# Kernel optimization log

Hardware: AMD Instinct MI355X
Metric: run time of the kernel (lower is better)

## Reference

```python
import jax, jax.numpy as jnp
import numpy as np

B, S, D, H = 4, 2048, 1024, 16
DK = D // H


def setup_inputs() -> dict:
    key = jax.random.key(0)
    ks = jax.random.split(key, 11)
    inp = {
        'query': jax.random.normal(ks[0], (B, S, D), jnp.float32),
        'key': jax.random.normal(ks[1], (B, S, D), jnp.float32),
        'value': jax.random.normal(ks[2], (B, S, D), jnp.float32),
        'mask': jnp.tril(jnp.ones((1, 1, S, S), dtype=bool)),  # causal
    }
    sc = 1.0 / np.sqrt(D)
    inp['w_q'] = jax.random.normal(ks[3], (D, D), jnp.float32) * sc
    inp['b_q'] = jnp.zeros((D,), jnp.float32)
    inp['w_k'] = jax.random.normal(ks[4], (D, D), jnp.float32) * sc
    inp['b_k'] = jnp.zeros((D,), jnp.float32)
    inp['w_v'] = jax.random.normal(ks[5], (D, D), jnp.float32) * sc
    inp['b_v'] = jnp.zeros((D,), jnp.float32)
    inp['w_o'] = jax.random.normal(ks[6], (D, D), jnp.float32) * sc
    inp['b_o'] = jnp.zeros((D,), jnp.float32)
    return inp


def _split_heads(x):
    # Faithful to source: view(B, S, d_k, H) then permute(0,3,1,2)
    b, s, _ = x.shape
    return x.reshape(b, s, DK, H).transpose(0, 3, 1, 2)  # (B, H, S, DK)


def _concat_heads(x):
    # permute(0,2,1,3) -> reshape(B, S, d_k*H)
    b, h, s, dk = x.shape
    return x.transpose(0, 2, 1, 3).reshape(b, s, dk * h)


def reference(query, key, value, mask, w_q, b_q, w_k, b_k, w_v, b_v, w_o, b_o):
    q = query @ w_q.T + b_q
    k = key @ w_k.T + b_k
    v = value @ w_v.T + b_v
    q, k, v = _split_heads(q), _split_heads(k), _split_heads(v)
    scale = 1.0 / jnp.sqrt(jnp.asarray(DK, q.dtype))
    scores = jnp.einsum('bhqd,bhkd->bhqk', q, k) * scale
    scores = jnp.where(mask, scores, -jnp.inf)
    attn = jax.nn.softmax(scores, axis=-1)  # dropout p=0 -> identity
    out = jnp.einsum('bhqk,bhkd->bhqd', attn, v)
    return _concat_heads(out) @ w_o.T + b_o
```

## Files before the change

### kernel.cpp

```cpp
#include <hip/hip_runtime.h>

#define BB 4
#define SS 2048
#define DD 1024
#define HH 16
#define DK 64
#define MM (BB * SS)

typedef __bf16 bf16x8 __attribute__((ext_vector_type(8)));
typedef float f32x4 __attribute__((ext_vector_type(4)));
typedef unsigned short us8 __attribute__((ext_vector_type(8)));
typedef unsigned short us4 __attribute__((ext_vector_type(4)));

#define MFMA_BF16(a, b, c) __builtin_amdgcn_mfma_f32_16x16x32_bf16((a), (b), (c), 0, 0, 0)

__device__ __forceinline__ unsigned short f2bf(float f) {
  return __builtin_bit_cast(unsigned short, (__bf16)f);
}

__device__ __forceinline__ bf16x8 ld_frag(const unsigned short* p) {
  return __builtin_bit_cast(bf16x8, *(const us8*)p);
}

__device__ __forceinline__ void gl_lds16(const unsigned short* g, unsigned short* l) {
  __builtin_amdgcn_global_load_lds((const __attribute__((address_space(1))) void*)g,
                                   (__attribute__((address_space(3))) void*)l, 16, 0, 0);
}

__global__ void cvt_weights(const float* __restrict__ w0, const float* __restrict__ w1,
                            const float* __restrict__ w2, const float* __restrict__ w3,
                            unsigned short* __restrict__ dst) {
  const float* src = (blockIdx.y == 0) ? w0 : (blockIdx.y == 1) ? w1 : (blockIdx.y == 2) ? w2 : w3;
  unsigned short* d = dst + (size_t)blockIdx.y * (DD * DD);
  int idx = (blockIdx.x * 256 + threadIdx.x) * 4;
  float4 v = *(const float4*)(src + idx);
  us4 o;
  o[0] = f2bf(v.x); o[1] = f2bf(v.y); o[2] = f2bf(v.z); o[3] = f2bf(v.w);
  *(us4*)(d + idx) = o;
}

__global__ __launch_bounds__(256, 3) void qkv_gemm(
    const float* __restrict__ xq, const float* __restrict__ xk, const float* __restrict__ xv,
    const unsigned short* __restrict__ wb,
    const float* __restrict__ bq, const float* __restrict__ bk, const float* __restrict__ bv,
    unsigned short* __restrict__ qh, unsigned short* __restrict__ kh,
    unsigned short* __restrict__ vt) {
  const int mode = blockIdx.z;
  const float* x = (mode == 0) ? xq : (mode == 1) ? xk : xv;
  const unsigned short* w = wb + (size_t)mode * (DD * DD);
  const float* bias = (mode == 0) ? bq : (mode == 1) ? bk : bv;

  const int m0 = blockIdx.x * 128;
  const int h0 = blockIdx.y * 2;

  __shared__ unsigned short smem[17408];
  unsigned short* sA = smem;
  unsigned short* sB = smem + 8192;

  const int tid = threadIdx.x;
  const int lane = tid & 63;
  const int wave = tid >> 6;
  const int wm = wave & 1, wn = wave >> 1;
  const int quad = lane >> 4, l16 = lane & 15;

  f32x4 acc[4][4];
#pragma unroll
  for (int i = 0; i < 4; i++)
#pragma unroll
    for (int j = 0; j < 4; j++) acc[i][j] = f32x4{0.f, 0.f, 0.f, 0.f};

  const int arow = tid >> 1, ahalf = tid & 1;
  const float* ag = x + (size_t)(m0 + arow) * DD + ahalf * 32;
  unsigned short* arow_base = sA + ahalf * 4096 + arow * 32;
  const int asw = (arow >> 1) & 3;

  const unsigned short* bsrc[4];
  unsigned short* bdst[4];
#pragma unroll
  for (int j = 0; j < 4; j++) {
    int cid = tid + j * 256;
    int half = cid >> 9, rr = (cid & 511) >> 2, c8 = (cid & 3) << 3;
    int n = ((rr & 63) << 4) + h0 + (rr >> 6);
    bsrc[j] = w + (size_t)n * DD + half * 32 + c8;
    bdst[j] = sB + half * 4096 + rr * 32 + c8;
  }

  float4 va[8];
  us8 vbr[4];
#pragma unroll
  for (int i = 0; i < 8; i++) va[i] = *(const float4*)(ag + 0 + i * 4);
#pragma unroll
  for (int j = 0; j < 4; j++) vbr[j] = *(const us8*)(bsrc[j] + 0);

  for (int k0 = 0; k0 < DD; k0 += 64) {
    __syncthreads();
#pragma unroll
    for (int c = 0; c < 4; c++) {
      us8 o;
      o[0] = f2bf(va[2 * c].x); o[1] = f2bf(va[2 * c].y);
      o[2] = f2bf(va[2 * c].z); o[3] = f2bf(va[2 * c].w);
      o[4] = f2bf(va[2 * c + 1].x); o[5] = f2bf(va[2 * c + 1].y);
      o[6] = f2bf(va[2 * c + 1].z); o[7] = f2bf(va[2 * c + 1].w);
      *(us8*)(arow_base + ((c ^ asw) << 3)) = o;
    }
#pragma unroll
    for (int j = 0; j < 4; j++) *(us8*)(bdst[j]) = vbr[j];
    __syncthreads();

    if (k0 + 64 < DD) {
#pragma unroll
      for (int i = 0; i < 8; i++) va[i] = *(const float4*)(ag + k0 + 64 + i * 4);
#pragma unroll
      for (int j = 0; j < 4; j++) vbr[j] = *(const us8*)(bsrc[j] + k0 + 64);
    }

#pragma unroll
    for (int kk = 0; kk < 2; kk++) {
      bf16x8 af[4];
#pragma unroll
      for (int mi = 0; mi < 4; mi++) {
        int row = wm * 64 + mi * 16 + l16;
        af[mi] = ld_frag(sA + kk * 4096 + row * 32 + ((quad ^ ((row >> 1) & 3)) << 3));
      }
#pragma unroll
      for (int ni = 0; ni < 4; ni++) {
        bf16x8 bfr = ld_frag(sB + kk * 4096 + (wn * 64 + ni * 16 + l16) * 32 + quad * 8);
#pragma unroll
        for (int mi = 0; mi < 4; mi++) acc[mi][ni] = MFMA_BF16(af[mi], bfr, acc[mi][ni]);
      }
    }
  }

  if (mode < 2) {
    unsigned short* outp = (mode == 0) ? qh : kh;
#pragma unroll
    for (int mi = 0; mi < 4; mi++) {
#pragma unroll
      for (int ni = 0; ni < 4; ni++) {
        int c = wn * 64 + ni * 16 + l16;
        int h = h0 + (c >> 6), dk = c & 63;
        float bvv = bias[(dk << 4) + h];
        int mg0 = m0 + wm * 64 + mi * 16 + quad * 4;
#pragma unroll
        for (int r = 0; r < 4; r++) {
          int mg = mg0 + r;
          int bb = mg >> 11, s = mg & 2047;
          size_t dst = ((size_t)((bb << 4) + h) * SS + s) * DK + dk;
          outp[dst] = f2bf(acc[mi][ni][r] + bvv);
        }
      }
    }
  } else {
    __syncthreads();
#pragma unroll
    for (int mi = 0; mi < 4; mi++) {
#pragma unroll
      for (int ni = 0; ni < 4; ni++) {
        int c = wn * 64 + ni * 16 + l16;
        int h = h0 + (c >> 6), dk = c & 63;
        float bvv = bias[(dk << 4) + h];
        int ml0 = wm * 64 + mi * 16 + quad * 4;
#pragma unroll
        for (int r = 0; r < 4; r++)
          smem[c * 136 + ml0 + r] = f2bf(acc[mi][ni][r] + bvv);
      }
    }
    __syncthreads();
    int bb = m0 >> 11;
    int sbase = m0 & 2047;
#pragma unroll
    for (int i = 0; i < 8; i++) {
      int idx = tid + i * 256;
      int c = idx >> 4, mc = (idx & 15) << 3;
      int h = h0 + (c >> 6), dk = c & 63;
      size_t dst = ((size_t)((bb << 4) + h) * DK + dk) * SS + sbase + mc;
      *(us8*)(vt + dst) = *(const us8*)(smem + c * 136 + mc);
    }
  }
}

__global__ __launch_bounds__(256, 2) void attn(
    const unsigned short* __restrict__ qh, const unsigned short* __restrict__ kh,
    const unsigned short* __restrict__ vt, unsigned short* __restrict__ outc) {
  const int bh = blockIdx.x;
  const int by = blockIdx.y;
  const int b = bh >> 4, h = bh & 15;
  const unsigned short* Qp = qh + (size_t)bh * SS * DK;
  const unsigned short* Kp = kh + (size_t)bh * SS * DK;
  const unsigned short* Vp = vt + (size_t)bh * DK * SS;

  __shared__ unsigned short sK[128 * 72];
  __shared__ unsigned short sV[64 * 136];

  const int tid = threadIdx.x;
  const int lane = tid & 63;
  const int wave = tid >> 6;
  const int quad = lane >> 4, l16 = lane & 15;
  const int wq0 = wave * 32;

  const float sl = 0.125f * 1.44269504088896f;

  for (int pass = 0; pass < 2; pass++) {
    const int qt = pass ? (15 - by) : by;
    const int q0 = qt * 128;

    bf16x8 aq[2][2];
#pragma unroll
    for (int mi = 0; mi < 2; mi++)
#pragma unroll
      for (int kk = 0; kk < 2; kk++)
        aq[mi][kk] = ld_frag(Qp + (size_t)(q0 + wq0 + mi * 16 + l16) * DK + kk * 32 + quad * 8);

    f32x4 o_acc[2][4];
    float mrowL[2], lrowL[2];
#pragma unroll
    for (int mi = 0; mi < 2; mi++) {
#pragma unroll
      for (int ni = 0; ni < 4; ni++) o_acc[mi][ni] = f32x4{0.f, 0.f, 0.f, 0.f};
      mrowL[mi] = -1e30f;
      lrowL[mi] = 0.f;
    }

    for (int kt = 0; kt <= qt; kt++) {
      const int k0 = kt * 128;
      const bool diag = (kt == qt);
      __syncthreads();
#pragma unroll
      for (int i = 0; i < 4; i++) {
        int idx = tid + i * 256;
        int row = idx >> 3, c8 = (idx & 7) << 3;
        *(us8*)(sK + row * 72 + c8) = *(const us8*)(Kp + (size_t)(k0 + row) * DK + c8);
      }
#pragma unroll
      for (int i = 0; i < 4; i++) {
        int idx = tid + i * 256;
        int row = idx >> 4, cc = (idx & 15) << 3;
        *(us8*)(sV + row * 136 + cc) = *(const us8*)(Vp + (size_t)row * SS + k0 + cc);
      }
      __syncthreads();

      f32x4 sc[2][8];
#pragma unroll
      for (int mi = 0; mi < 2; mi++)
#pragma unroll
        for (int kti = 0; kti < 8; kti++) sc[mi][kti] = f32x4{0.f, 0.f, 0.f, 0.f};
#pragma unroll
      for (int kti = 0; kti < 8; kti++) {
#pragma unroll
        for (int kk = 0; kk < 2; kk++) {
          bf16x8 ak = ld_frag(sK + (kti * 16 + l16) * 72 + kk * 32 + quad * 8);
#pragma unroll
          for (int mi = 0; mi < 2; mi++) sc[mi][kti] = MFMA_BF16(ak, aq[mi][kk], sc[mi][kti]);
        }
      }

      if (diag) {
#pragma unroll
        for (int mi = 0; mi < 2; mi++) {
          int ql = wq0 + mi * 16 + l16;
#pragma unroll
          for (int kti = 0; kti < 8; kti++)
#pragma unroll
            for (int r = 0; r < 4; r++) {
              int kl = kti * 16 + quad * 4 + r;
              float v = sc[mi][kti][r] * sl;
              sc[mi][kti][r] = (kl > ql) ? -1e30f : v;
            }
        }
      } else {
#pragma unroll
        for (int mi = 0; mi < 2; mi++)
#pragma unroll
          for (int kti = 0; kti < 8; kti++)
#pragma unroll
            for (int r = 0; r < 4; r++) sc[mi][kti][r] *= sl;
      }

      float alphaL[2];
#pragma unroll
      for (int mi = 0; mi < 2; mi++) {
        f32x4 vm = sc[mi][0];
#pragma unroll
        for (int kti = 1; kti < 8; kti++)
#pragma unroll
          for (int r = 0; r < 4; r++) vm[r] = fmaxf(vm[r], sc[mi][kti][r]);
        float mx = fmaxf(fmaxf(vm[0], vm[1]), fmaxf(vm[2], vm[3]));
        mx = fmaxf(mx, __shfl_xor(mx, 16, 64));
        mx = fmaxf(mx, __shfl_xor(mx, 32, 64));
        float mnew = fmaxf(mrowL[mi], mx);
        alphaL[mi] = exp2f(mrowL[mi] - mnew);
        mrowL[mi] = mnew;
      }

#pragma unroll
      for (int mi = 0; mi < 2; mi++) {
#pragma unroll
        for (int r = 0; r < 4; r++) {
          float a = __shfl(alphaL[mi], quad * 4 + r, 64);
#pragma unroll
          for (int ni = 0; ni < 4; ni++) o_acc[mi][ni][r] *= a;
        }
        us4 pk[8];
        f32x4 vs = f32x4{0.f, 0.f, 0.f, 0.f};
#pragma unroll
        for (int kti = 0; kti < 8; kti++) {
#pragma unroll
          for (int r = 0; r < 4; r++) {
            float p = exp2f(sc[mi][kti][r] - mrowL[mi]);
            vs[r] += p;
            pk[kti][r] = f2bf(p);
          }
        }
        float ls = (vs[0] + vs[1]) + (vs[2] + vs[3]);
        ls += __shfl_xor(ls, 16, 64);
        ls += __shfl_xor(ls, 32, 64);
        lrowL[mi] = lrowL[mi] * alphaL[mi] + ls;

#pragma unroll
        for (int c = 0; c < 4; c++) {
          bf16x8 ap = __builtin_bit_cast(
              bf16x8, __builtin_shufflevector(pk[2 * c], pk[2 * c + 1], 0, 1, 2, 3, 4, 5, 6, 7));
#pragma unroll
          for (int ni = 0; ni < 4; ni++) {
            const unsigned short* vb = sV + (ni * 16 + l16) * 136 + c * 32 + quad * 4;
            us4 lo = *(const us4*)vb;
            us4 hi = *(const us4*)(vb + 16);
            bf16x8 bfr = __builtin_bit_cast(
                bf16x8, __builtin_shufflevector(lo, hi, 0, 1, 2, 3, 4, 5, 6, 7));
            o_acc[mi][ni] = MFMA_BF16(ap, bfr, o_acc[mi][ni]);
          }
        }
      }
    }

#pragma unroll
    for (int mi = 0; mi < 2; mi++) {
#pragma unroll
      for (int r = 0; r < 4; r++) {
        float lr = __shfl(lrowL[mi], quad * 4 + r, 64);
        float inv = 1.0f / lr;
        int qg = q0 + wq0 + mi * 16 + quad * 4 + r;
        size_t rowbase = ((size_t)(b * SS + qg)) * DD + h * DK;
#pragma unroll
        for (int ni = 0; ni < 4; ni++) {
          int dk = ni * 16 + l16;
          outc[rowbase + dk] = f2bf(o_acc[mi][ni][r] * inv);
        }
      }
    }
    __syncthreads();
  }
}

__global__ __launch_bounds__(256, 4) void out_proj(
    const unsigned short* __restrict__ ac, const unsigned short* __restrict__ wo,
    const float* __restrict__ bias, float* __restrict__ out) {
  const int m0 = blockIdx.x * 128;
  const int n0 = blockIdx.y * 128;
  __shared__ unsigned short sA[8192];
  __shared__ unsigned short sB[8192];

  const int tid = threadIdx.x;
  const int lane = tid & 63;
  const int wave = tid >> 6;
  const int wm = wave & 1, wn = wave >> 1;
  const int quad = lane >> 4, l16 = lane & 15;

  f32x4 acc[4][4];
#pragma unroll
  for (int i = 0; i < 4; i++)
#pragma unroll
    for (int j = 0; j < 4; j++) acc[i][j] = f32x4{0.f, 0.f, 0.f, 0.f};

  for (int k0 = 0; k0 < DD; k0 += 64) {
    __syncthreads();
#pragma unroll
    for (int j = 0; j < 4; j++) {
      int cid = tid + j * 256;
      int half = cid >> 9;
      int rr = (cid & 511) >> 2;
      int c8 = (cid & 3) << 3;
      gl_lds16(ac + (size_t)(m0 + rr) * DD + k0 + half * 32 + c8,
               sA + half * 4096 + rr * 32 + c8);
    }
#pragma unroll
    for (int j = 0; j < 4; j++) {
      int cid = tid + j * 256;
      int half = cid >> 9;
      int rr = (cid & 511) >> 2;
      int c8 = (cid & 3) << 3;
      gl_lds16(wo + (size_t)(n0 + rr) * DD + k0 + half * 32 + c8,
               sB + half * 4096 + rr * 32 + c8);
    }
    __syncthreads();
#pragma unroll
    for (int kk = 0; kk < 2; kk++) {
      bf16x8 af[4];
#pragma unroll
      for (int mi = 0; mi < 4; mi++)
        af[mi] = ld_frag(sA + kk * 4096 + (wm * 64 + mi * 16 + l16) * 32 + quad * 8);
#pragma unroll
      for (int ni = 0; ni < 4; ni++) {
        bf16x8 bfr = ld_frag(sB + kk * 4096 + (wn * 64 + ni * 16 + l16) * 32 + quad * 8);
#pragma unroll
        for (int mi = 0; mi < 4; mi++) acc[mi][ni] = MFMA_BF16(af[mi], bfr, acc[mi][ni]);
      }
    }
  }

#pragma unroll
  for (int mi = 0; mi < 4; mi++) {
#pragma unroll
    for (int ni = 0; ni < 4; ni++) {
      int n = n0 + wn * 64 + ni * 16 + l16;
      float bvv = bias[n];
      int mg0 = m0 + wm * 64 + mi * 16 + quad * 4;
#pragma unroll
      for (int r = 0; r < 4; r++) out[(size_t)(mg0 + r) * DD + n] = acc[mi][ni][r] + bvv;
    }
  }
}

extern "C" void kernel_launch(void* const* d_in, const int* in_sizes, int n_in,
                              void* d_out, int out_size, void* d_ws, size_t ws_size,
                              hipStream_t stream) {
  const float* q_in = (const float*)d_in[0];
  const float* k_in = (const float*)d_in[1];
  const float* v_in = (const float*)d_in[2];
  const float* w_q = (const float*)d_in[4];
  const float* b_q = (const float*)d_in[5];
  const float* w_k = (const float*)d_in[6];
  const float* b_k = (const float*)d_in[7];
  const float* w_v = (const float*)d_in[8];
  const float* b_v = (const float*)d_in[9];
  const float* w_o = (const float*)d_in[10];
  const float* b_o = (const float*)d_in[11];
  float* out = (float*)d_out;

  unsigned short* ws = (unsigned short*)d_ws;
  unsigned short* wb = ws;
  unsigned short* qh = ws + (size_t)4 * 1024 * 1024;
  unsigned short* kh = ws + (size_t)12 * 1024 * 1024;
  unsigned short* vt = ws + (size_t)20 * 1024 * 1024;
  unsigned short* outc = ws + (size_t)28 * 1024 * 1024;

  const size_t WSZ = (size_t)DD * DD;

  cvt_weights<<<dim3(1024, 4), 256, 0, stream>>>(w_q, w_k, w_v, w_o, wb);
  qkv_gemm<<<dim3(64, 8, 3), 256, 0, stream>>>(q_in, k_in, v_in, wb, b_q, b_k, b_v, qh, kh, vt);
  attn<<<dim3(64, 8), 256, 0, stream>>>(qh, kh, vt, outc);
  out_proj<<<dim3(64, 8), 256, 0, stream>>>(outc, wb + 3 * WSZ, b_o, out);
}
```

Measured before the change: 371.1 us.

## Pre-convert activations to bf16 and load QKV tiles via global_load_lds

Adds a separate kernel that converts the fp32 query/key/value activations to bf16 in workspace buffers, then splits the fused QKV GEMM into three launches that stream bf16 tiles directly into LDS with global_load_lds. This removes the in-loop fp32-to-bf16 conversion and the register staging, but it drops the register prefetch overlap and the LDS swizzle, so bank conflicts and load latency may become exposed. Workspace regions are reused for the converted activations, ordered safely by the sequence of launches on one stream. It also adds s_setprio around the MFMA blocks in attention to favour matrix issue.

```diff
diff --git a/kernel.cpp b/kernel.cpp
--- a/kernel.cpp
+++ b/kernel.cpp
@@ -39,17 +39,23 @@
   *(us4*)(d + idx) = o;
 }
 
-__global__ __launch_bounds__(256, 3) void qkv_gemm(
-    const float* __restrict__ xq, const float* __restrict__ xk, const float* __restrict__ xv,
-    const unsigned short* __restrict__ wb,
-    const float* __restrict__ bq, const float* __restrict__ bk, const float* __restrict__ bv,
-    unsigned short* __restrict__ qh, unsigned short* __restrict__ kh,
-    unsigned short* __restrict__ vt) {
-  const int mode = blockIdx.z;
-  const float* x = (mode == 0) ? xq : (mode == 1) ? xk : xv;
-  const unsigned short* w = wb + (size_t)mode * (DD * DD);
-  const float* bias = (mode == 0) ? bq : (mode == 1) ? bk : bv;
-
+__global__ void cvt_act(const float* __restrict__ xq, const float* __restrict__ xk,
+                        const float* __restrict__ xv, unsigned short* __restrict__ dq,
+                        unsigned short* __restrict__ dk, unsigned short* __restrict__ dv) {
+  const float* src = (blockIdx.y == 0) ? xq : (blockIdx.y == 1) ? xk : xv;
+  unsigned short* dst = (blockIdx.y == 0) ? dq : (blockIdx.y == 1) ? dk : dv;
+  int idx = (blockIdx.x * 256 + threadIdx.x) * 8;
+  float4 a = *(const float4*)(src + idx);
+  float4 b = *(const float4*)(src + idx + 4);
+  us8 o;
+  o[0] = f2bf(a.x); o[1] = f2bf(a.y); o[2] = f2bf(a.z); o[3] = f2bf(a.w);
+  o[4] = f2bf(b.x); o[5] = f2bf(b.y); o[6] = f2bf(b.z); o[7] = f2bf(b.w);
+  *(us8*)(dst + idx) = o;
+}
+
+__global__ __launch_bounds__(256, 4) void qkv_gemm_bf(
+    const unsigned short* __restrict__ xb, const unsigned short* __restrict__ w,
+    const float* __restrict__ bias, unsigned short* __restrict__ outp, int mode) {
   const int m0 = blockIdx.x * 128;
   const int h0 = blockIdx.y * 2;
 
@@ -69,59 +75,31 @@
 #pragma unroll
     for (int j = 0; j < 4; j++) acc[i][j] = f32x4{0.f, 0.f, 0.f, 0.f};
 
-  const int arow = tid >> 1, ahalf = tid & 1;
-  const float* ag = x + (size_t)(m0 + arow) * DD + ahalf * 32;
-  unsigned short* arow_base = sA + ahalf * 4096 + arow * 32;
-  const int asw = (arow >> 1) & 3;
-
-  const unsigned short* bsrc[4];
-  unsigned short* bdst[4];
-#pragma unroll
-  for (int j = 0; j < 4; j++) {
-    int cid = tid + j * 256;
-    int half = cid >> 9, rr = (cid & 511) >> 2, c8 = (cid & 3) << 3;
-    int n = ((rr & 63) << 4) + h0 + (rr >> 6);
-    bsrc[j] = w + (size_t)n * DD + half * 32 + c8;
-    bdst[j] = sB + half * 4096 + rr * 32 + c8;
-  }
-
-  float4 va[8];
-  us8 vbr[4];
-#pragma unroll
-  for (int i = 0; i < 8; i++) va[i] = *(const float4*)(ag + 0 + i * 4);
-#pragma unroll
-  for (int j = 0; j < 4; j++) vbr[j] = *(const us8*)(bsrc[j] + 0);
-
   for (int k0 = 0; k0 < DD; k0 += 64) {
     __syncthreads();
 #pragma unroll
-    for (int c = 0; c < 4; c++) {
-      us8 o;
-      o[0] = f2bf(va[2 * c].x); o[1] = f2bf(va[2 * c].y);
-      o[2] = f2bf(va[2 * c].z); o[3] = f2bf(va[2 * c].w);
-      o[4] = f2bf(va[2 * c + 1].x); o[5] = f2bf(va[2 * c + 1].y);
-      o[6] = f2bf(va[2 * c + 1].z); o[7] = f2bf(va[2 * c + 1].w);
-      *(us8*)(arow_base + ((c ^ asw) << 3)) = o;
-    }
-#pragma unroll
-    for (int j = 0; j < 4; j++) *(us8*)(bdst[j]) = vbr[j];
-    __syncthreads();
-
-    if (k0 + 64 < DD) {
-#pragma unroll
-      for (int i = 0; i < 8; i++) va[i] = *(const float4*)(ag + k0 + 64 + i * 4);
-#pragma unroll
-      for (int j = 0; j < 4; j++) vbr[j] = *(const us8*)(bsrc[j] + k0 + 64);
-    }
+    for (int j = 0; j < 4; j++) {
+      int cid = tid + j * 256;
+      int half = cid >> 9, rr = (cid & 511) >> 2, c8 = (cid & 3) << 3;
+      gl_lds16(xb + (size_t)(m0 + rr) * DD + k0 + half * 32 + c8,
+               sA + half * 4096 + rr * 32 + c8);
+    }
+#pragma unroll
+    for (int j = 0; j < 4; j++) {
+      int cid = tid + j * 256;
+      int half = cid >> 9, rr = (cid & 511) >> 2, c8 = (cid & 3) << 3;
+      int n = ((rr & 63) << 4) + h0 + (rr >> 6);
+      gl_lds16(w + (size_t)n * DD + k0 + half * 32 + c8,
+               sB + half * 4096 + rr * 32 + c8);
+    }
+    __syncthreads();
 
 #pragma unroll
     for (int kk = 0; kk < 2; kk++) {
       bf16x8 af[4];
 #pragma unroll
-      for (int mi = 0; mi < 4; mi++) {
-        int row = wm * 64 + mi * 16 + l16;
-        af[mi] = ld_frag(sA + kk * 4096 + row * 32 + ((quad ^ ((row >> 1) & 3)) << 3));
-      }
+      for (int mi = 0; mi < 4; mi++)
+        af[mi] = ld_frag(sA + kk * 4096 + (wm * 64 + mi * 16 + l16) * 32 + quad * 8);
 #pragma unroll
       for (int ni = 0; ni < 4; ni++) {
         bf16x8 bfr = ld_frag(sB + kk * 4096 + (wn * 64 + ni * 16 + l16) * 32 + quad * 8);
@@ -132,7 +110,6 @@
   }
 
   if (mode < 2) {
-    unsigned short* outp = (mode == 0) ? qh : kh;
 #pragma unroll
     for (int mi = 0; mi < 4; mi++) {
 #pragma unroll
@@ -174,7 +151,7 @@
       int c = idx >> 4, mc = (idx & 15) << 3;
       int h = h0 + (c >> 6), dk = c & 63;
       size_t dst = ((size_t)((bb << 4) + h) * DK + dk) * SS + sbase + mc;
-      *(us8*)(vt + dst) = *(const us8*)(smem + c * 136 + mc);
+      *(us8*)(outp + dst) = *(const us8*)(smem + c * 136 + mc);
     }
   }
 }
@@ -244,6 +221,7 @@
       for (int mi = 0; mi < 2; mi++)
 #pragma unroll
         for (int kti = 0; kti < 8; kti++) sc[mi][kti] = f32x4{0.f, 0.f, 0.f, 0.f};
+      __builtin_amdgcn_s_setprio(1);
 #pragma unroll
       for (int kti = 0; kti < 8; kti++) {
 #pragma unroll
@@ -253,6 +231,7 @@
           for (int mi = 0; mi < 2; mi++) sc[mi][kti] = MFMA_BF16(ak, aq[mi][kk], sc[mi][kti]);
         }
       }
+      __builtin_amdgcn_s_setprio(0);
 
       if (diag) {
 #pragma unroll
@@ -316,6 +295,7 @@
         ls += __shfl_xor(ls, 32, 64);
         lrowL[mi] = lrowL[mi] * alphaL[mi] + ls;
 
+        __builtin_amdgcn_s_setprio(1);
 #pragma unroll
         for (int c = 0; c < 4; c++) {
           bf16x8 ap = __builtin_bit_cast(
@@ -330,6 +310,7 @@
             o_acc[mi][ni] = MFMA_BF16(ap, bfr, o_acc[mi][ni]);
           }
         }
+        __builtin_amdgcn_s_setprio(0);
       }
     }
 
@@ -443,11 +424,17 @@
   unsigned short* kh = ws + (size_t)12 * 1024 * 1024;
   unsigned short* vt = ws + (size_t)20 * 1024 * 1024;
   unsigned short* outc = ws + (size_t)28 * 1024 * 1024;
+  unsigned short* xqb = kh;
+  unsigned short* xkb = vt;
+  unsigned short* xvb = outc;
 
   const size_t WSZ = (size_t)DD * DD;
 
   cvt_weights<<<dim3(1024, 4), 256, 0, stream>>>(w_q, w_k, w_v, w_o, wb);
-  qkv_gemm<<<dim3(64, 8, 3), 256, 0, stream>>>(q_in, k_in, v_in, wb, b_q, b_k, b_v, qh, kh, vt);
+  cvt_act<<<dim3(4096, 3), 256, 0, stream>>>(q_in, k_in, v_in, xqb, xkb, xvb);
+  qkv_gemm_bf<<<dim3(64, 8), 256, 0, stream>>>(xqb, wb, b_q, qh, 0);
+  qkv_gemm_bf<<<dim3(64, 8), 256, 0, stream>>>(xkb, wb + WSZ, b_k, kh, 1);
+  qkv_gemm_bf<<<dim3(64, 8), 256, 0, stream>>>(xvb, wb + 2 * WSZ, b_v, vt, 2);
   attn<<<dim3(64, 8), 256, 0, stream>>>(qh, kh, vt, outc);
   out_proj<<<dim3(64, 8), 256, 0, stream>>>(outc, wb + 3 * WSZ, b_o, out);
 }
```

Result: faster. 362.7 us (-2.2%).
